# Performance work log

Measured on AMD Instinct MI355X. Metric: run time of the kernel, lower is better.

Reference implementation:

```python
import jax, jax.numpy as jnp
import numpy as np

NEG_SLOPE = 0.2


def gat_conv(x, src, dst, W, a_src, a_dst, bias, heads, out_ch):
    # x: [N, F_in]; src/dst: [E] (message flows src -> dst, softmax over dst)
    N = x.shape[0]
    h = (x @ W).reshape(N, heads, out_ch)              # [N, H, C]
    alpha_s = (h * a_src).sum(-1)                      # [N, H]
    alpha_d = (h * a_dst).sum(-1)                      # [N, H]
    e = jax.nn.leaky_relu(alpha_s[src] + alpha_d[dst], NEG_SLOPE)  # [E, H]
    # segment softmax over destination nodes (every node has a self loop)
    emax = jax.ops.segment_max(e, dst, num_segments=N)             # [N, H]
    ee = jnp.exp(e - emax[dst])
    denom = jax.ops.segment_sum(ee, dst, num_segments=N)           # [N, H]
    alpha = ee / denom[dst]                                        # [E, H]
    msg = h[src] * alpha[..., None]                                # [E, H, C]
    out = jax.ops.segment_sum(msg, dst, num_segments=N)            # [N, H, C]
    return out.reshape(N, heads * out_ch) + bias


def setup_inputs() -> dict:
    key = jax.random.key(0)
    ks = jax.random.split(key, 12)
    N, E, EL = 100000, 1600000, 100000
    F_in, C, H = 128, 64, 2
    glorot = lambda k, shp: jax.random.normal(k, shp, jnp.float32) * np.sqrt(2.0 / (shp[0] + shp[-1]))
    return {
        "x": jax.random.normal(ks[0], (N, F_in), jnp.float32),
        "edge_index": jax.random.randint(ks[1], (2, E), 0, N, jnp.int32),
        "edge_label_index": jax.random.randint(ks[2], (2, EL), 0, N, jnp.int32),
        "W1": glorot(ks[3], (F_in, H * C)),
        "a_src1": glorot(ks[4], (H, C)),
        "a_dst1": glorot(ks[5], (H, C)),
        "b1": jnp.zeros((H * C,), jnp.float32),
        "W2": glorot(ks[6], (H * C, C)),
        "a_src2": glorot(ks[7], (1, C)),
        "a_dst2": glorot(ks[8], (1, C)),
        "b2": jnp.zeros((C,), jnp.float32),
    }


def reference(x, edge_index, edge_label_index, W1, a_src1, a_dst1, b1, W2, a_src2, a_dst2, b2):
    N = x.shape[0]
    # add self loops (PyG GATConv default)
    loop = jnp.arange(N, dtype=edge_index.dtype)
    src = jnp.concatenate([edge_index[0], loop])
    dst = jnp.concatenate([edge_index[1], loop])
    H, C = a_src1.shape[0], a_src1.shape[1]
    z = jax.nn.elu(gat_conv(x, src, dst, W1, a_src1, a_dst1, b1, H, C))
    z = gat_conv(z, src, dst, W2, a_src2, a_dst2, b2, 1, C)         # [N, C]
    # decode: dot product of endpoint embeddings
    return (z[edge_label_index[0]] * z[edge_label_index[1]]).sum(axis=1)
```

## Files before the change

kernel.cpp:

```cpp
#include <hip/hip_runtime.h>
#include <hip/hip_bf16.h>

#define NEG_SLOPE 0.2f
#define LRELU(v) ((v) > 0.f ? (v) : NEG_SLOPE * (v))
#define BBITS 7
#define BSZ 128

typedef unsigned short ushort_t;
typedef unsigned int uint_t;
typedef float v2f __attribute__((ext_vector_type(2)));
typedef float f32x4 __attribute__((ext_vector_type(4)));
typedef short bf16x8 __attribute__((ext_vector_type(8)));

static inline int cdiv(int a, int b) { return (a + b - 1) / b; }

__device__ __forceinline__ float wsum(float v) {
#pragma unroll
    for (int o = 32; o; o >>= 1) v += __shfl_xor(v, o);
    return v;
}
__device__ __forceinline__ ushort_t f2bfbits(float f) {
    __hip_bfloat16 b = __float2bfloat16(f);
    return *reinterpret_cast<ushort_t*>(&b);
}

__global__ __launch_bounds__(256) void k_zero_int(int* p, int n) {
    int i = blockIdx.x * 256 + threadIdx.x;
    if (i < n) p[i] = 0;
}

__global__ __launch_bounds__(256) void k_bhist(const int* __restrict__ ei, int E, int ET, int NB,
                                               int* __restrict__ bcnt) {
    extern __shared__ int hist[];
    for (int i = threadIdx.x; i < NB; i += 256) hist[i] = 0;
    __syncthreads();
    int stride = gridDim.x * 256;
    for (int i = blockIdx.x * 256 + threadIdx.x; i < ET; i += stride) {
        int d = (i < E) ? ei[E + i] : (i - E);
        atomicAdd(&hist[d >> BBITS], 1);
    }
    __syncthreads();
    for (int i = threadIdx.x; i < NB; i += 256) {
        int c = hist[i];
        if (c) atomicAdd(&bcnt[i], c);
    }
}

__global__ void k_scan_small(const int* __restrict__ bcnt, int NB,
                             int* __restrict__ boff, int* __restrict__ bcur,
                             int* __restrict__ offs, int N, int ET) {
    extern __shared__ int sm[];
    for (int i = threadIdx.x; i < NB; i += blockDim.x) sm[i] = bcnt[i];
    __syncthreads();
    if (threadIdx.x == 0) {
        int run = 0;
        for (int i = 0; i < NB; i++) { int c = sm[i]; sm[i] = run; run += c; }
    }
    __syncthreads();
    for (int i = threadIdx.x; i < NB; i += blockDim.x) { boff[i] = sm[i]; bcur[i] = sm[i]; }
    if (threadIdx.x == 0) { boff[NB] = ET; offs[N] = ET; }
}

__global__ __launch_bounds__(256) void k_bscatter(const int* __restrict__ ei, int E, int ET, int NB,
                                                  int* __restrict__ bcur,
                                                  long long* __restrict__ tmp) {
    extern __shared__ int sm2[];
    int* hist = sm2;
    int* cur = sm2 + NB;
    const int CH = 4096;
    int c0 = blockIdx.x * CH;
    int c1 = min(ET, c0 + CH);
    for (int i = threadIdx.x; i < NB; i += 256) hist[i] = 0;
    __syncthreads();
    for (int i = c0 + threadIdx.x; i < c1; i += 256) {
        int d = (i < E) ? ei[E + i] : (i - E);
        atomicAdd(&hist[d >> BBITS], 1);
    }
    __syncthreads();
    for (int i = threadIdx.x; i < NB; i += 256) {
        int c = hist[i];
        cur[i] = c ? atomicAdd(&bcur[i], c) : 0;
    }
    __syncthreads();
    for (int i = c0 + threadIdx.x; i < c1; i += 256) {
        int s = (i < E) ? ei[i] : (i - E);
        int d = (i < E) ? ei[E + i] : (i - E);
        int pos = atomicAdd(&cur[d >> BBITS], 1);
        tmp[pos] = ((long long)d << 32) | (unsigned)s;
    }
}

__global__ __launch_bounds__(256) void k_csrfin(const long long* __restrict__ tmp,
                                                const int* __restrict__ boff, int NB, int N,
                                                int* __restrict__ offs, int* __restrict__ ssrc) {
    __shared__ int deg[BSZ], cur[BSZ], sc[BSZ];
    int b = blockIdx.x;
    int node0 = b << BBITS;
    int nn = min(BSZ, N - node0);
    int r0 = boff[b], r1 = boff[b + 1];
    int t = threadIdx.x;
    if (t < BSZ) deg[t] = 0;
    __syncthreads();
    for (int i = r0 + t; i < r1; i += 256) {
        int d = (int)(tmp[i] >> 32);
        atomicAdd(&deg[d - node0], 1);
    }
    __syncthreads();
    if (t < BSZ) sc[t] = deg[t];
    __syncthreads();
    for (int o = 1; o < BSZ; o <<= 1) {
        int v = 0;
        if (t < BSZ && t >= o) v = sc[t - o];
        __syncthreads();
        if (t < BSZ) sc[t] += v;
        __syncthreads();
    }
    if (t < BSZ) {
        int ex = sc[t] - deg[t];
        cur[t] = r0 + ex;
        if (t < nn) offs[node0 + t] = r0 + ex;
    }
    __syncthreads();
    for (int i = r0 + t; i < r1; i += 256) {
        long long v = tmp[i];
        int d = (int)(v >> 32);
        int s = (int)(v & 0xffffffffLL);
        int pos = atomicAdd(&cur[d - node0], 1);
        ssrc[pos] = s;
    }
}

__global__ __launch_bounds__(256) void k_wt(const float* __restrict__ W, ushort_t* __restrict__ Wt,
                                            int K, int M) {
    for (int idx = blockIdx.x * 256 + threadIdx.x; idx < K * M; idx += gridDim.x * 256) {
        int k = idx / M, n = idx % M;
        Wt[n * K + k] = f2bfbits(W[idx]);
    }
}

template <int M, int H>
__global__ __launch_bounds__(256) void k_gemm_mfma(const float* __restrict__ x,
                                                   const ushort_t* __restrict__ Wt,
                                                   const float* __restrict__ a_src,
                                                   const float* __restrict__ a_dst,
                                                   ushort_t* __restrict__ h,
                                                   float* __restrict__ as, float* __restrict__ ad,
                                                   int N) {
    constexpr int T = M / 16;
    int t = threadIdx.x;
    int w = t >> 6;
    int lane = t & 63;
    int ln = lane & 15;
    int q = lane >> 4;
    int rowA = blockIdx.x * 64 + w * 16 + ln;
    int rowD0 = blockIdx.x * 64 + w * 16 + q * 4;

    f32x4 acc[T];
#pragma unroll
    for (int i = 0; i < T; i++) acc[i] = (f32x4){0.f, 0.f, 0.f, 0.f};

#pragma unroll
    for (int kc = 0; kc < 4; kc++) {
        bf16x8 afrag;
        float xv[8];
        if (rowA < N) {
            float4 v0 = *(const float4*)(x + (size_t)rowA * 128 + kc * 32 + q * 8);
            float4 v1 = *(const float4*)(x + (size_t)rowA * 128 + kc * 32 + q * 8 + 4);
            xv[0] = v0.x; xv[1] = v0.y; xv[2] = v0.z; xv[3] = v0.w;
            xv[4] = v1.x; xv[5] = v1.y; xv[6] = v1.z; xv[7] = v1.w;
        } else {
#pragma unroll
            for (int j = 0; j < 8; j++) xv[j] = 0.f;
        }
#pragma unroll
        for (int j = 0; j < 8; j++) afrag[j] = (short)f2bfbits(xv[j]);
#pragma unroll
        for (int tt = 0; tt < T; tt++) {
            bf16x8 bfrag = *(const bf16x8*)(Wt + (size_t)(tt * 16 + ln) * 128 + kc * 32 + q * 8);
            acc[tt] = __builtin_amdgcn_mfma_f32_16x16x32_bf16(afrag, bfrag, acc[tt], 0, 0, 0);
        }
    }

#pragma unroll
    for (int tt = 0; tt < T; tt++)
#pragma unroll
        for (int r = 0; r < 4; r++) {
            int row = rowD0 + r;
            if (row < N) h[(size_t)row * M + tt * 16 + ln] = f2bfbits(acc[tt][r]);
        }

    float avs[T], avd[T];
#pragma unroll
    for (int tt = 0; tt < T; tt++) {
        avs[tt] = a_src[tt * 16 + ln];
        avd[tt] = a_dst[tt * 16 + ln];
    }
#pragma unroll
    for (int r = 0; r < 4; r++) {
        int row = rowD0 + r;
        if (H == 2) {
            float ps0 = 0.f, ps1 = 0.f, pd0 = 0.f, pd1 = 0.f;
#pragma unroll
            for (int tt = 0; tt < T / 2; tt++) { ps0 += acc[tt][r] * avs[tt]; pd0 += acc[tt][r] * avd[tt]; }
#pragma unroll
            for (int tt = T / 2; tt < T; tt++) { ps1 += acc[tt][r] * avs[tt]; pd1 += acc[tt][r] * avd[tt]; }
#pragma unroll
            for (int o = 8; o; o >>= 1) {
                ps0 += __shfl_down(ps0, o, 16); pd0 += __shfl_down(pd0, o, 16);
                ps1 += __shfl_down(ps1, o, 16); pd1 += __shfl_down(pd1, o, 16);
            }
            if (ln == 0 && row < N) {
                as[(size_t)row * 2] = ps0; as[(size_t)row * 2 + 1] = ps1;
                ad[(size_t)row * 2] = pd0; ad[(size_t)row * 2 + 1] = pd1;
            }
        } else {
            float ps = 0.f, pd = 0.f;
#pragma unroll
            for (int tt = 0; tt < T; tt++) { ps += acc[tt][r] * avs[tt]; pd += acc[tt][r] * avd[tt]; }
#pragma unroll
            for (int o = 8; o; o >>= 1) {
                ps += __shfl_down(ps, o, 16); pd += __shfl_down(pd, o, 16);
            }
            if (ln == 0 && row < N) { as[row] = ps; ad[row] = pd; }
        }
    }
}

template <int H, bool ELU_ACT>
__global__ __launch_bounds__(256) void k_agg_fused(const int* __restrict__ offs,
                                                   const int* __restrict__ ssrc,
                                                   const ushort_t* __restrict__ h,
                                                   const float* __restrict__ as,
                                                   const float* __restrict__ ad,
                                                   const float* __restrict__ bias,
                                                   float* __restrict__ z, int N) {
    constexpr int G = 8 * H;
    constexpr int EPW = 64 / G;
    constexpr int NBG = 4;
    constexpr int RB = H * 128;
    __shared__ float pl[4][64 * H];
    int d = (blockIdx.x * 256 + threadIdx.x) >> 6;
    int lane = threadIdx.x & 63;
    float* pw = pl[threadIdx.x >> 6];
    if (d >= N) return;
    int cpos = lane % G;
    int sub = lane / G;
    int hself = (H == 2) ? (cpos >> 3) : 0;
    const char* hb = (const char*)h;

    float adh[H], den[H];
#pragma unroll
    for (int hh = 0; hh < H; hh++) { adh[hh] = ad[(size_t)d * H + hh]; den[hh] = 0.f; }
    v2f acc2[4];
#pragma unroll
    for (int i = 0; i < 4; i++) acc2[i] = (v2f){0.f, 0.f};

    int e0 = offs[d], e1 = offs[d + 1];
    for (int cb = e0; cb < e1; cb += 64) {
        int ne = min(64, e1 - cb);
        unsigned so = 0;
        float p[H];
#pragma unroll
        for (int hh = 0; hh < H; hh++) p[hh] = 0.f;
        if (lane < ne) {
            int s_l = ssrc[cb + lane];
            so = (unsigned)s_l * RB;
            if (H == 2) {
                float2 av = ((const float2*)as)[s_l];
                p[0] = __expf(LRELU(av.x + adh[0]));
                p[1] = __expf(LRELU(av.y + adh[1]));
            } else {
                p[0] = __expf(LRELU(as[s_l] + adh[0]));
            }
        }
#pragma unroll
        for (int hh = 0; hh < H; hh++) den[hh] += wsum(p[hh]);
        if (H == 2) {
            pw[lane * 2] = p[0];
            pw[lane * 2 + 1] = p[1];
        } else {
            pw[lane] = p[0];
        }
        for (int j = 0; j < ne; j += NBG * EPW) {
            uint4 hv[NBG];
            int el[NBG];
            bool ok[NBG];
#pragma unroll
            for (int g = 0; g < NBG; g++) {
                int eidx = j + g * EPW + sub;
                el[g] = eidx & 63;
                ok[g] = eidx < ne;
                unsigned so_e = (unsigned)__shfl((int)so, el[g]);
                hv[g] = make_uint4(0u, 0u, 0u, 0u);
                if (ok[g]) hv[g] = *(const uint4*)(hb + (so_e + cpos * 16));
            }
#pragma unroll
            for (int g = 0; g < NBG; g++) {
                float pvs = ok[g] ? pw[el[g] * H + hself] : 0.f;
                v2f pv = {pvs, pvs};
                v2f t0 = {__uint_as_float(hv[g].x << 16), __uint_as_float(hv[g].x & 0xffff0000u)};
                v2f t1 = {__uint_as_float(hv[g].y << 16), __uint_as_float(hv[g].y & 0xffff0000u)};
                v2f t2 = {__uint_as_float(hv[g].z << 16), __uint_as_float(hv[g].z & 0xffff0000u)};
                v2f t3 = {__uint_as_float(hv[g].w << 16), __uint_as_float(hv[g].w & 0xffff0000u)};
                acc2[0] += pv * t0;
                acc2[1] += pv * t1;
                acc2[2] += pv * t2;
                acc2[3] += pv * t3;
            }
        }
    }
#pragma unroll
    for (int o = G; o < 64; o <<= 1)
#pragma unroll
        for (int i = 0; i < 4; i++) {
            acc2[i][0] += __shfl_xor(acc2[i][0], o);
            acc2[i][1] += __shfl_xor(acc2[i][1], o);
        }
    if (lane < G) {
        float inv = 1.f / ((H == 2 && hself) ? den[1] : den[0]);
        float vout[8];
#pragma unroll
        for (int i = 0; i < 4; i++) {
            vout[2 * i] = acc2[i][0] * inv + bias[cpos * 8 + 2 * i];
            vout[2 * i + 1] = acc2[i][1] * inv + bias[cpos * 8 + 2 * i + 1];
        }
        if (ELU_ACT) {
#pragma unroll
            for (int i = 0; i < 8; i++) vout[i] = vout[i] > 0.f ? vout[i] : expm1f(vout[i]);
        }
        float* zp = z + (size_t)d * (H * 64) + cpos * 8;
        *(float4*)zp = make_float4(vout[0], vout[1], vout[2], vout[3]);
        *(float4*)(zp + 4) = make_float4(vout[4], vout[5], vout[6], vout[7]);
    }
}

__global__ __launch_bounds__(256) void k_decode(const int* __restrict__ eli,
                                                const float* __restrict__ z,
                                                float* __restrict__ out, int EL) {
    int wid = (blockIdx.x * 256 + threadIdx.x) >> 6;
    int lane = threadIdx.x & 63;
    int pi = wid * 2 + (lane >> 5);
    if (pi >= EL) return;
    int hl = lane & 31;
    int a = eli[pi], b = eli[EL + pi];
    float2 za = ((const float2*)(z + (size_t)a * 64))[hl];
    float2 zb = ((const float2*)(z + (size_t)b * 64))[hl];
    float p = za.x * zb.x + za.y * zb.y;
#pragma unroll
    for (int o = 16; o; o >>= 1) p += __shfl_down(p, o, 32);
    if (hl == 0) out[pi] = p;
}

extern "C" void kernel_launch(void* const* d_in, const int* in_sizes, int n_in,
                              void* d_out, int out_size, void* d_ws, size_t ws_size,
                              hipStream_t stream) {
    const float* x   = (const float*)d_in[0];
    const int*   ei  = (const int*)d_in[1];
    const int*   eli = (const int*)d_in[2];
    const float* W1  = (const float*)d_in[3];
    const float* as1 = (const float*)d_in[4];
    const float* ad1 = (const float*)d_in[5];
    const float* b1  = (const float*)d_in[6];
    const float* W2  = (const float*)d_in[7];
    const float* as2 = (const float*)d_in[8];
    const float* ad2 = (const float*)d_in[9];
    const float* b2  = (const float*)d_in[10];

    int N  = in_sizes[0] / 128;
    int E  = in_sizes[1] / 2;
    int EL = in_sizes[2] / 2;
    int ET = E + N;
    int NB = cdiv(N, BSZ);

    char* ws = (char*)d_ws;
    size_t off = 0;
    auto alloc = [&](size_t nbytes) -> void* {
        void* p = ws + off;
        off += (nbytes + 255) & ~(size_t)255;
        return p;
    };
    ushort_t* Hbuf = (ushort_t*)alloc((size_t)N * 128 * 2);
    float*    Zbuf = (float*)alloc((size_t)N * 128 * 4);
    float*    AS   = (float*)alloc((size_t)N * 2 * 4);
    float*    AD   = (float*)alloc((size_t)N * 2 * 4);
    int*      OFF  = (int*)alloc((size_t)(N + 1) * 4);
    int*      SSRC = (int*)alloc((size_t)ET * 4);
    int*      BCNT = (int*)alloc((size_t)NB * 4);
    int*      BOFF = (int*)alloc((size_t)(NB + 1) * 4);
    int*      BCUR = (int*)alloc((size_t)NB * 4);
    ushort_t* WT1  = (ushort_t*)alloc(128 * 128 * 2);
    ushort_t* WT2  = (ushort_t*)alloc(64 * 128 * 2);
    long long* TMP = (long long*)Zbuf;

    k_zero_int<<<cdiv(NB, 256), 256, 0, stream>>>(BCNT, NB);
    k_bhist<<<256, 256, NB * 4, stream>>>(ei, E, ET, NB, BCNT);
    k_scan_small<<<1, 256, NB * 4, stream>>>(BCNT, NB, BOFF, BCUR, OFF, N, ET);
    k_bscatter<<<cdiv(ET, 4096), 256, 2 * NB * 4, stream>>>(ei, E, ET, NB, BCUR, TMP);
    k_csrfin<<<NB, 256, 0, stream>>>(TMP, BOFF, NB, N, OFF, SSRC);

    k_wt<<<32, 256, 0, stream>>>(W1, WT1, 128, 128);
    k_wt<<<16, 256, 0, stream>>>(W2, WT2, 128, 64);

    k_gemm_mfma<128, 2><<<cdiv(N, 64), 256, 0, stream>>>(x, WT1, as1, ad1, Hbuf, AS, AD, N);
    k_agg_fused<2, true><<<cdiv(N, 4), 256, 0, stream>>>(OFF, SSRC, Hbuf, AS, AD, b1, Zbuf, N);

    k_gemm_mfma<64, 1><<<cdiv(N, 64), 256, 0, stream>>>(Zbuf, WT2, as2, ad2, Hbuf, AS, AD, N);
    k_agg_fused<1, false><<<cdiv(N, 4), 256, 0, stream>>>(OFF, SSRC, Hbuf, AS, AD, b2, Zbuf, N);

    k_decode<<<cdiv(EL, 8), 256, 0, stream>>>(eli, Zbuf, (float*)d_out, EL);
}
```

Before: 372.5 us.

## Split each gathered row across twice the lanes and stage edge metadata in LDS

In the fused aggregation kernel, each feature row is now covered by 16*H lanes, each loading 8 bytes instead of 16, so fewer edges are handled per wave step. The per-edge source offset and attention weight are written together to LDS as one record. They are read back directly, which replaces the per-edge shuffle, the bounds masks and the separate weight lookup. Out-of-range slots hold a zero weight and offset zero, so no predication is needed. The trade-off is narrower loads per lane and more loop iterations per edge chunk.

Measured after the change: 365.1 us. 2.0% less time.

```diff
diff --git a/kernel.cpp b/kernel.cpp
--- a/kernel.cpp
+++ b/kernel.cpp
@@ -234,26 +234,28 @@
                                                    const float* __restrict__ ad,
                                                    const float* __restrict__ bias,
                                                    float* __restrict__ z, int N) {
-    constexpr int G = 8 * H;
+    constexpr int G = 16 * H;
     constexpr int EPW = 64 / G;
-    constexpr int NBG = 4;
     constexpr int RB = H * 128;
-    __shared__ float pl[4][64 * H];
+    __shared__ uint2 meta[4][64 * H];
+    int wv = threadIdx.x >> 6;
+    int lane = threadIdx.x & 63;
     int d = (blockIdx.x * 256 + threadIdx.x) >> 6;
-    int lane = threadIdx.x & 63;
-    float* pw = pl[threadIdx.x >> 6];
     if (d >= N) return;
+    uint2* mw = meta[wv];
     int cpos = lane % G;
     int sub = lane / G;
-    int hself = (H == 2) ? (cpos >> 3) : 0;
+    int hself = (H == 2) ? (cpos >> 4) : 0;
     const char* hb = (const char*)h;
+    int cpo8 = cpos * 8;
+    const char* mbase = (const char*)mw + ((H == 2) ? (sub * 16 + hself * 8) : (sub * 8));
 
     float adh[H], den[H];
 #pragma unroll
     for (int hh = 0; hh < H; hh++) { adh[hh] = ad[(size_t)d * H + hh]; den[hh] = 0.f; }
-    v2f acc2[4];
-#pragma unroll
-    for (int i = 0; i < 4; i++) acc2[i] = (v2f){0.f, 0.f};
+    v2f acc2[2];
+    acc2[0] = (v2f){0.f, 0.f};
+    acc2[1] = (v2f){0.f, 0.f};
 
     int e0 = offs[d], e1 = offs[d + 1];
     for (int cb = e0; cb < e1; cb += 64) {
@@ -276,61 +278,50 @@
 #pragma unroll
         for (int hh = 0; hh < H; hh++) den[hh] += wsum(p[hh]);
         if (H == 2) {
-            pw[lane * 2] = p[0];
-            pw[lane * 2 + 1] = p[1];
+            ((uint4*)mw)[lane] =
+                make_uint4(so, __float_as_uint(p[0]), so, __float_as_uint(p[1]));
         } else {
-            pw[lane] = p[0];
-        }
-        for (int j = 0; j < ne; j += NBG * EPW) {
-            uint4 hv[NBG];
-            int el[NBG];
-            bool ok[NBG];
-#pragma unroll
-            for (int g = 0; g < NBG; g++) {
-                int eidx = j + g * EPW + sub;
-                el[g] = eidx & 63;
-                ok[g] = eidx < ne;
-                unsigned so_e = (unsigned)__shfl((int)so, el[g]);
-                hv[g] = make_uint4(0u, 0u, 0u, 0u);
-                if (ok[g]) hv[g] = *(const uint4*)(hb + (so_e + cpos * 16));
-            }
-#pragma unroll
-            for (int g = 0; g < NBG; g++) {
-                float pvs = ok[g] ? pw[el[g] * H + hself] : 0.f;
+            mw[lane] = make_uint2(so, __float_as_uint(p[0]));
+        }
+        int ng = (ne + EPW - 1) / EPW;
+        for (int g0 = 0; g0 < ng; g0 += 4) {
+            uint2 m[4];
+#pragma unroll
+            for (int g = 0; g < 4; g++) m[g] = *(const uint2*)(mbase + (g0 + g) * 32);
+            uint2 hv[4];
+#pragma unroll
+            for (int g = 0; g < 4; g++) hv[g] = *(const uint2*)(hb + (m[g].x + cpo8));
+#pragma unroll
+            for (int g = 0; g < 4; g++) {
+                float pvs = __uint_as_float(m[g].y);
                 v2f pv = {pvs, pvs};
                 v2f t0 = {__uint_as_float(hv[g].x << 16), __uint_as_float(hv[g].x & 0xffff0000u)};
                 v2f t1 = {__uint_as_float(hv[g].y << 16), __uint_as_float(hv[g].y & 0xffff0000u)};
-                v2f t2 = {__uint_as_float(hv[g].z << 16), __uint_as_float(hv[g].z & 0xffff0000u)};
-                v2f t3 = {__uint_as_float(hv[g].w << 16), __uint_as_float(hv[g].w & 0xffff0000u)};
                 acc2[0] += pv * t0;
                 acc2[1] += pv * t1;
-                acc2[2] += pv * t2;
-                acc2[3] += pv * t3;
             }
         }
     }
 #pragma unroll
-    for (int o = G; o < 64; o <<= 1)
-#pragma unroll
-        for (int i = 0; i < 4; i++) {
-            acc2[i][0] += __shfl_xor(acc2[i][0], o);
-            acc2[i][1] += __shfl_xor(acc2[i][1], o);
-        }
+    for (int o = G; o < 64; o <<= 1) {
+        acc2[0][0] += __shfl_xor(acc2[0][0], o);
+        acc2[0][1] += __shfl_xor(acc2[0][1], o);
+        acc2[1][0] += __shfl_xor(acc2[1][0], o);
+        acc2[1][1] += __shfl_xor(acc2[1][1], o);
+    }
     if (lane < G) {
         float inv = 1.f / ((H == 2 && hself) ? den[1] : den[0]);
-        float vout[8];
-#pragma unroll
-        for (int i = 0; i < 4; i++) {
-            vout[2 * i] = acc2[i][0] * inv + bias[cpos * 8 + 2 * i];
-            vout[2 * i + 1] = acc2[i][1] * inv + bias[cpos * 8 + 2 * i + 1];
-        }
+        float vout[4];
+        vout[0] = acc2[0][0] * inv + bias[cpos * 4 + 0];
+        vout[1] = acc2[0][1] * inv + bias[cpos * 4 + 1];
+        vout[2] = acc2[1][0] * inv + bias[cpos * 4 + 2];
+        vout[3] = acc2[1][1] * inv + bias[cpos * 4 + 3];
         if (ELU_ACT) {
 #pragma unroll
-            for (int i = 0; i < 8; i++) vout[i] = vout[i] > 0.f ? vout[i] : expm1f(vout[i]);
-        }
-        float* zp = z + (size_t)d * (H * 64) + cpos * 8;
-        *(float4*)zp = make_float4(vout[0], vout[1], vout[2], vout[3]);
-        *(float4*)(zp + 4) = make_float4(vout[4], vout[5], vout[6], vout[7]);
+            for (int i = 0; i < 4; i++) vout[i] = vout[i] > 0.f ? vout[i] : expm1f(vout[i]);
+        }
+        *(float4*)(z + (size_t)d * (H * 64) + cpos * 4) =
+            make_float4(vout[0], vout[1], vout[2], vout[3]);
     }
 }
 
```
